# Performance work log

Hardware: AMD Instinct MI355X
Metric: run time of the kernel (lower is better)

## Reference

```python
import jax, jax.numpy as jnp
import numpy as np

EPS = 1e-8
E, H, F, MCL, V = 256, 512, 100, 500, 128000
CTX = MCL - 1  # encoder facts; decoder appends the mean-fact row
NUM_FACTS = 300


def setup_inputs() -> dict:
    key = jax.random.key(0)
    ks = jax.random.split(key, 16)

    def nrm(k, shape, s=0.02):
        return (jax.random.normal(k, shape) * s).astype(jnp.float32)

    return {
        "context": jax.random.randint(ks[0], (CTX, F), 0, V),
        "word_emb": nrm(ks[1], (V, E)),
        "attn1_W": nrm(ks[2], (MCL, E + H)),
        "attn1_b": nrm(ks[3], (MCL,)),
        "attn2_W": nrm(ks[4], (1, MCL)),
        "attn2_b": nrm(ks[5], (1,)),
        "W_ih": nrm(ks[6], (3 * H, 2 * E + F)),
        "W_hh": nrm(ks[7], (3 * H, H)),
        "b_ih": nrm(ks[8], (3 * H,)),
        "b_hh": nrm(ks[9], (3 * H,)),
        "out1_W": nrm(ks[10], (H, E + H)),
        "out1_b": nrm(ks[11], (H,)),
        "out2_W": nrm(ks[12], (V, H)),
        "out2_b": nrm(ks[13], (V,)),
        "h0": jnp.zeros((1, 1, H), jnp.float32),
        "num_facts": NUM_FACTS,
    }


def _encode(context, word_emb):
    # EncoderModule: embedding lookup + PositionalFactEncoder
    emb = word_emb[context]  # [CTX, F, E]
    s = jnp.arange(F, dtype=jnp.float32) / (F - 1)  # slen axis
    e = jnp.arange(E, dtype=jnp.float32) / (E - 1)  # elen axis
    l = 1.0 - s[:, None] - e[None, :] * (1.0 - 2.0 * s[:, None])  # [F, E]
    return jnp.sum(emb * l[None], axis=1)  # [CTX, E]


def reference(context, word_emb, attn1_W, attn1_b, attn2_W, attn2_b,
              W_ih, W_hh, b_ih, b_hh, out1_W, out1_b, out2_W, out2_b,
              h0, num_facts):
    facts = _encode(context, word_emb)  # [CTX, E]
    mean_fact = jnp.mean(facts[:num_facts], axis=0, keepdims=True)  # [1, E]
    fact_embeddings = jnp.concatenate([facts, mean_fact], axis=0)  # [MCL, E]

    # fact-level attention
    h = jnp.broadcast_to(h0.reshape(1, H), (MCL, H))
    attn_in = jnp.concatenate([fact_embeddings, h], axis=1)  # [MCL, E+H]
    e1 = jnp.tanh(attn_in @ attn1_W.T + attn1_b)  # [MCL, MCL]
    energy = (e1 @ attn2_W.T + attn2_b).reshape(1, -1)  # [1, MCL]
    aw = jax.nn.softmax(energy, axis=1)

    # mask: first num_facts ones, zeros, then 1 for the mean/generate slot
    idx = jnp.arange(MCL)
    mask = jnp.where((idx < num_facts) | (idx == MCL - 1), 1.0, 0.0)[None, :]
    aw = aw * mask + EPS
    aw = aw / jnp.sum(aw)
    log_aw = jnp.log(aw)  # [1, MCL]

    attn_weighted_facts = aw @ fact_embeddings  # [1, E]
    f_max_idx = jnp.argmax(aw, axis=1)[0]
    emb_f_max = fact_embeddings[f_max_idx].reshape(1, E)

    # decoder input: embedding of token 1 + zero positional input
    dec_word = word_emb[1].reshape(1, E)
    dec_pos = jnp.zeros((1, F), jnp.float32)
    x = jnp.concatenate([dec_word, dec_pos, emb_f_max], axis=1)  # [1, 2E+F]

    # torch GRU cell (gates ordered r, z, n)
    hprev = h0.reshape(1, H)
    gi = x @ W_ih.T + b_ih
    gh = hprev @ W_hh.T + b_hh
    r = jax.nn.sigmoid(gi[:, :H] + gh[:, :H])
    z = jax.nn.sigmoid(gi[:, H:2 * H] + gh[:, H:2 * H])
    n = jnp.tanh(gi[:, 2 * H:] + r * gh[:, 2 * H:])
    h_new = (1.0 - z) * n + z * hprev  # [1, H]

    # generate branch (f_t == max_context_len - 1): vocab head
    out = jnp.concatenate([h_new, attn_weighted_facts], axis=1)  # [1, H+E]
    out = jax.nn.relu(out @ out1_W.T + out1_b)
    logits = out @ out2_W.T + out2_b  # [1, V]
    y_pred = jax.nn.log_softmax(logits, axis=1)

    decoder_hidden = h_new.reshape(1, 1, H)
    return y_pred, log_aw, decoder_hidden
```

## Files before the change

kernel.cpp:

```cpp
#include <hip/hip_runtime.h>
#include <math.h>

#define E_    256
#define H_    512
#define F_    100
#define MCL_  500
#define CTX_  499
#define V_    128000
#define EPS_  1e-8f

typedef float f4v __attribute__((ext_vector_type(4)));

#define WS_FE      0
#define WS_ENERGY  (WS_FE + MCL_*E_)
#define WS_EBIAS   (WS_ENERGY + MCL_)
#define WS_AWF     (WS_EBIAS + MCL_)
#define WS_FMAX    (WS_AWF + E_)
#define WS_HNEW    (WS_FMAX + E_)
#define WS_ACT     (WS_HNEW + H_)
#define WS_LOGITS  (WS_ACT + H_)
#define WS_BSUM    (WS_LOGITS + V_)
#define WS_CNT     (WS_BSUM + 1024)

__device__ __forceinline__ float wred64(float v) {
#pragma unroll
  for (int o = 32; o; o >>= 1) v += __shfl_xor(v, o, 64);
  return v;
}
__device__ __forceinline__ float qred16(float v) {
#pragma unroll
  for (int o = 8; o; o >>= 1) v += __shfl_xor(v, o, 64);
  return v;
}
__device__ __forceinline__ float dot4(float4 a, float4 b) {
  return a.x*b.x + a.y*b.y + a.z*b.z + a.w*b.w;
}
__device__ __forceinline__ float dot4v(f4v a, f4v b) {
  return a.x*b.x + a.y*b.y + a.z*b.z + a.w*b.w;
}

__global__ __launch_bounds__(256) void k_encode(const int* __restrict__ ctx,
                                                const float* __restrict__ wemb,
                                                float* __restrict__ fe,
                                                const float* __restrict__ a1W,
                                                const float* __restrict__ a1b,
                                                const float* __restrict__ h0,
                                                float* __restrict__ ebias,
                                                int* __restrict__ cnt) {
  __shared__ int toks[2][F_];
  const int t = threadIdx.x;
  if (blockIdx.x >= 250) {
    const int lane = t & 63, sub = lane & 15, grp = lane >> 4;
    const int wid = (blockIdx.x - 250) * 4 + (t >> 6);
    const float4* h4 = (const float4*)h0;
    float4 hr[8];
#pragma unroll
    for (int q = 0; q < 8; ++q) hr[q] = h4[sub + q * 16];
    for (int j0 = wid * 4; j0 < MCL_; j0 += 32 * 4) {
      const int j = j0 + grp;
      if (j < MCL_) {
        const float4* w4 = (const float4*)(a1W + (size_t)j * (E_ + H_) + E_);
        float acc = 0.f;
#pragma unroll
        for (int q = 0; q < 8; ++q) acc += dot4(w4[sub + q * 16], hr[q]);
        acc = qred16(acc);
        if (sub == 0) ebias[j] = acc + a1b[j];
      }
    }
    return;
  }
  if (blockIdx.x == 0 && t == 0) *cnt = 0;
  const int i0 = blockIdx.x * 2;
  const int i1 = i0 + 1;
  if (t < F_) toks[0][t] = ctx[i0 * F_ + t];
  else if (t < 2 * F_) toks[1][t - F_] = (i1 < CTX_) ? ctx[i1 * F_ + (t - F_)] : 0;
  __syncthreads();
  const int row = t >> 7, tt = t & 127;
  const int i = i0 + row;
  const float e0n = (2 * tt) * (1.0f / 255.0f);
  const float e1n = (2 * tt + 1) * (1.0f / 255.0f);
  float x0 = 0.f, y0 = 0.f, x1 = 0.f, y1 = 0.f, x2 = 0.f, y2 = 0.f, x3 = 0.f, y3 = 0.f;
#pragma unroll 5
  for (int f = 0; f < F_; f += 4) {
#pragma unroll
    for (int u = 0; u < 4; ++u) {
      float s = (f + u) * (1.0f / 99.0f);
      float A = 1.0f - s, B = 1.0f - 2.0f * s;
      float l0 = A - e0n * B, l1 = A - e1n * B;
      float2 v = ((const float2*)(wemb + (size_t)toks[row][f + u] * E_))[tt];
      if (u == 0)      { x0 = fmaf(v.x, l0, x0); y0 = fmaf(v.y, l1, y0); }
      else if (u == 1) { x1 = fmaf(v.x, l0, x1); y1 = fmaf(v.y, l1, y1); }
      else if (u == 2) { x2 = fmaf(v.x, l0, x2); y2 = fmaf(v.y, l1, y2); }
      else             { x3 = fmaf(v.x, l0, x3); y3 = fmaf(v.y, l1, y3); }
    }
  }
  if (i < CTX_) {
    float2 r; r.x = (x0 + x1) + (x2 + x3); r.y = (y0 + y1) + (y2 + y3);
    ((float2*)(fe + (size_t)i * E_))[tt] = r;
  }
}

__global__ __launch_bounds__(256) void k_energy(float* __restrict__ fe,
                                                const float* __restrict__ a1W,
                                                const float* __restrict__ ebias,
                                                const float* __restrict__ a2W,
                                                const float* __restrict__ a2b,
                                                const int* __restrict__ nfp,
                                                float* __restrict__ energy,
                                                float* __restrict__ awf,
                                                float* __restrict__ fmaxrow,
                                                float* __restrict__ out_logaw,
                                                int* __restrict__ cnt) {
  __shared__ float sfe[4][E_];
  __shared__ float sred[4][256];
  __shared__ float saw[512];
  __shared__ int sticket;
  const int t = threadIdx.x;
  const int i0 = blockIdx.x * 4;
  const int nf = *nfp;

  if (blockIdx.x == 124) {
    float s0 = 0.f, s1 = 0.f, s2 = 0.f, s3 = 0.f;
    int i = 0;
    for (; i + 4 <= nf; i += 4) {
      s0 += fe[(i + 0) * E_ + t]; s1 += fe[(i + 1) * E_ + t];
      s2 += fe[(i + 2) * E_ + t]; s3 += fe[(i + 3) * E_ + t];
    }
    for (; i < nf; ++i) s0 += fe[i * E_ + t];
    float mv = ((s0 + s1) + (s2 + s3)) / (float)nf;
    sfe[3][t] = mv;
    fe[CTX_ * E_ + t] = mv;
    sfe[0][t] = fe[496 * E_ + t];
    sfe[1][t] = fe[497 * E_ + t];
    sfe[2][t] = fe[498 * E_ + t];
  } else {
#pragma unroll
    for (int r = 0; r < 4; ++r) sfe[r][t] = fe[(i0 + r) * E_ + t];
  }
  __syncthreads();
  float c0 = 0.f, c1 = 0.f, c2 = 0.f, c3 = 0.f;
  const float4* s0p = (const float4*)sfe[0];
  const float4* s1p = (const float4*)sfe[1];
  const float4* s2p = (const float4*)sfe[2];
  const float4* s3p = (const float4*)sfe[3];
  for (int j = t; j < MCL_; j += 256) {
    const float4* w4 = (const float4*)(a1W + (size_t)j * (E_ + H_));
    float d0 = 0.f, d1 = 0.f, d2 = 0.f, d3 = 0.f;
#pragma unroll 8
    for (int q = 0; q < E_ / 4; ++q) {
      float4 a = w4[q];
      d0 += dot4(a, s0p[q]);
      d1 += dot4(a, s1p[q]);
      d2 += dot4(a, s2p[q]);
      d3 += dot4(a, s3p[q]);
    }
    float bj = ebias[j], wj = a2W[j];
    c0 = fmaf(wj, tanhf(d0 + bj), c0);
    c1 = fmaf(wj, tanhf(d1 + bj), c1);
    c2 = fmaf(wj, tanhf(d2 + bj), c2);
    c3 = fmaf(wj, tanhf(d3 + bj), c3);
  }
  sred[0][t] = c0; sred[1][t] = c1; sred[2][t] = c2; sred[3][t] = c3;
  __syncthreads();
  for (int s = 128; s; s >>= 1) {
    if (t < s) {
#pragma unroll
      for (int r = 0; r < 4; ++r) sred[r][t] += sred[r][t + s];
    }
    __syncthreads();
  }
  if (t < 4) energy[i0 + t] = sred[t][0] + a2b[0];

  __threadfence();
  if (t == 0) sticket = atomicAdd(cnt, 1);
  __syncthreads();
  if (sticket != 124) return;
  __threadfence();

  float* red = sred[0];
  int* idx = (int*)sred[1];
  float ev0 = energy[t];
  float ev1 = (t + 256 < MCL_) ? energy[t + 256] : -1e30f;
  red[t] = fmaxf(ev0, ev1); __syncthreads();
  for (int s = 128; s; s >>= 1) { if (t < s) red[t] = fmaxf(red[t], red[t + s]); __syncthreads(); }
  const float mx = red[0]; __syncthreads();

  float p0 = __expf(ev0 - mx);
  float p1 = (t + 256 < MCL_) ? __expf(ev1 - mx) : 0.f;
  red[t] = p0 + p1; __syncthreads();
  for (int s = 128; s; s >>= 1) { if (t < s) red[t] += red[t + s]; __syncthreads(); }
  const float S1 = red[0]; __syncthreads();

  float m0 = ((t < nf) || (t == MCL_ - 1)) ? 1.f : 0.f;
  float m1 = (((t + 256) < nf) || ((t + 256) == MCL_ - 1)) ? 1.f : 0.f;
  float a0 = p0 / S1 * m0 + EPS_;
  float a1 = (t + 256 < MCL_) ? (p1 / S1 * m1 + EPS_) : 0.f;
  red[t] = a0 + a1; __syncthreads();
  for (int s = 128; s; s >>= 1) { if (t < s) red[t] += red[t + s]; __syncthreads(); }
  const float S2 = red[0]; __syncthreads();

  a0 /= S2; a1 /= S2;
  out_logaw[t] = logf(a0);
  if (t + 256 < MCL_) out_logaw[t + 256] = logf(a1);
  saw[t] = a0;
  saw[t + 256] = (t + 256 < MCL_) ? a1 : 0.f;

  float bv; int bi;
  if ((t + 256 < MCL_) && (a1 > a0)) { bv = a1; bi = t + 256; } else { bv = a0; bi = t; }
  red[t] = bv; idx[t] = bi; __syncthreads();
  for (int s = 128; s; s >>= 1) {
    if (t < s) {
      float o = red[t + s]; int oi = idx[t + s];
      if (o > red[t] || (o == red[t] && oi < idx[t])) { red[t] = o; idx[t] = oi; }
    }
    __syncthreads();
  }
  const int fidx = idx[0]; __syncthreads();

  float pa = 0.f, pb = 0.f;
  for (int i2 = 0; i2 < MCL_; i2 += 2) {
    pa = fmaf(saw[i2], fe[i2 * E_ + t], pa);
    pb = fmaf(saw[i2 + 1], fe[(i2 + 1) * E_ + t], pb);
  }
  awf[t] = pa + pb;
  fmaxrow[t] = fe[fidx * E_ + t];
}

__global__ __launch_bounds__(256) void k_gates_gru(const float* __restrict__ Wih,
                                                   const float* __restrict__ bih,
                                                   const float* __restrict__ Whh,
                                                   const float* __restrict__ bhh,
                                                   const float* __restrict__ wemb,
                                                   const float* __restrict__ fmaxrow,
                                                   const float* __restrict__ h0,
                                                   float* __restrict__ hnew,
                                                   float* __restrict__ out_hidden) {
  const int t = threadIdx.x, lane = t & 63, w = t >> 6;
  const int h = blockIdx.x * 4 + w;
  const float4* xa4 = (const float4*)(wemb + E_);
  const float4* xb4 = (const float4*)fmaxrow;
  const float4* h4  = (const float4*)h0;
  float4 xav = xa4[lane], xbv = xb4[lane];
  float4 hva = h4[lane], hvb = h4[lane + 64];
  const float* rr = Wih + (size_t)h * (2 * E_ + F_);
  const float* rz = Wih + (size_t)(H_ + h) * (2 * E_ + F_);
  const float* rn = Wih + (size_t)(2 * H_ + h) * (2 * E_ + F_);
  float gir = dot4(((const float4*)rr)[lane], xav) + dot4(((const float4*)(rr + E_ + F_))[lane], xbv);
  float giz = dot4(((const float4*)rz)[lane], xav) + dot4(((const float4*)(rz + E_ + F_))[lane], xbv);
  float gin = dot4(((const float4*)rn)[lane], xav) + dot4(((const float4*)(rn + E_ + F_))[lane], xbv);
  const float4* wr = (const float4*)(Whh + (size_t)h * H_);
  const float4* wz = (const float4*)(Whh + (size_t)(H_ + h) * H_);
  const float4* wn = (const float4*)(Whh + (size_t)(2 * H_ + h) * H_);
  float ghr = dot4(wr[lane], hva) + dot4(wr[lane + 64], hvb);
  float ghz = dot4(wz[lane], hva) + dot4(wz[lane + 64], hvb);
  float ghn = dot4(wn[lane], hva) + dot4(wn[lane + 64], hvb);
  gir = wred64(gir); giz = wred64(giz); gin = wred64(gin);
  ghr = wred64(ghr); ghz = wred64(ghz); ghn = wred64(ghn);
  if (lane == 0) {
    float r = 1.f / (1.f + __expf(-(gir + bih[h] + ghr + bhh[h])));
    float z = 1.f / (1.f + __expf(-(giz + bih[H_ + h] + ghz + bhh[H_ + h])));
    float n = tanhf(gin + bih[2 * H_ + h] + r * (ghn + bhh[2 * H_ + h]));
    float hv = (1.f - z) * n + z * h0[h];
    hnew[h] = hv;
    out_hidden[h] = hv;
  }
}

__global__ __launch_bounds__(256) void k_out1(const float* __restrict__ o1W,
                                              const float* __restrict__ o1b,
                                              const float* __restrict__ hnew,
                                              const float* __restrict__ awf,
                                              float* __restrict__ act) {
  __shared__ float cat[H_ + E_];
  const int t = threadIdx.x;
#pragma unroll
  for (int idx = t; idx < H_; idx += 256) cat[idx] = hnew[idx];
  cat[H_ + t] = awf[t];
  __syncthreads();
  const int lane = t & 63, sub = lane & 15, grp = lane >> 4;
  const int gw = blockIdx.x * 4 + (t >> 6);
  const float4* c4 = (const float4*)cat;
  const int r = gw * 4 + grp;
  const float4* w4 = (const float4*)(o1W + (size_t)r * (H_ + E_));
  float acc = 0.f;
#pragma unroll
  for (int q = 0; q < 12; ++q) acc += dot4(w4[sub + q * 16], c4[sub + q * 16]);
  acc = qred16(acc);
  if (sub == 0) act[r] = fmaxf(acc + o1b[r], 0.f);
}

__global__ __launch_bounds__(256) void k_vocab(const float* __restrict__ o2W,
                                               const float* __restrict__ o2b,
                                               const float* __restrict__ act,
                                               float* __restrict__ logits,
                                               float* __restrict__ bsum) {
  __shared__ float swsum[4];
  const int t = threadIdx.x;
  const int lane = t & 63, sub = lane & 15, grp = lane >> 4, w = t >> 6;
  const int gw = blockIdx.x * 4 + w;
  const int nW = 1024 * 4;
  const f4v* a4 = (const f4v*)act;
  f4v ar[8];
#pragma unroll
  for (int q = 0; q < 8; ++q) ar[q] = a4[sub + q * 16];
  float sumexp = 0.f;
  for (int v0 = gw * 8; v0 < V_; v0 += nW * 8) {
    const int vA = v0 + grp;
    const int vB = v0 + 4 + grp;
    float accA = 0.f, accB = 0.f;
    if (vB < V_) {
      const f4v* wa = (const f4v*)(o2W + (size_t)vA * H_);
      const f4v* wb = (const f4v*)(o2W + (size_t)vB * H_);
      f4v la[8], lb[8];
#pragma unroll
      for (int q = 0; q < 8; ++q) la[q] = __builtin_nontemporal_load(&wa[sub + q * 16]);
#pragma unroll
      for (int q = 0; q < 8; ++q) lb[q] = __builtin_nontemporal_load(&wb[sub + q * 16]);
#pragma unroll
      for (int q = 0; q < 8; ++q) { accA += dot4v(la[q], ar[q]); accB += dot4v(lb[q], ar[q]); }
    } else if (vA < V_) {
      const f4v* wa = (const f4v*)(o2W + (size_t)vA * H_);
      f4v la[8];
#pragma unroll
      for (int q = 0; q < 8; ++q) la[q] = __builtin_nontemporal_load(&wa[sub + q * 16]);
#pragma unroll
      for (int q = 0; q < 8; ++q) accA += dot4v(la[q], ar[q]);
    }
    accA = qred16(accA);
    accB = qred16(accB);
    if (sub == 0) {
      if (vA < V_) { float lg = accA + o2b[vA]; logits[vA] = lg; sumexp += __expf(lg); }
      if (vB < V_) { float lg = accB + o2b[vB]; logits[vB] = lg; sumexp += __expf(lg); }
    }
  }
  sumexp = wred64(sumexp);
  if (lane == 0) swsum[w] = sumexp;
  __syncthreads();
  if (t == 0) bsum[blockIdx.x] = swsum[0] + swsum[1] + swsum[2] + swsum[3];
}

__global__ __launch_bounds__(256) void k_final(const float* __restrict__ logits,
                                               const float* __restrict__ bsum,
                                               float* __restrict__ y) {
  __shared__ float sr[256];
  const int t = threadIdx.x;
  float s = bsum[t] + bsum[t + 256] + bsum[t + 512] + bsum[t + 768];
  sr[t] = s; __syncthreads();
  for (int o = 128; o; o >>= 1) { if (t < o) sr[t] += sr[t + o]; __syncthreads(); }
  const float lz = logf(sr[0]);
  const int i = blockIdx.x * 256 + t;
  float4 l = ((const float4*)logits)[i];
  ((float4*)y)[i] = make_float4(l.x - lz, l.y - lz, l.z - lz, l.w - lz);
}

extern "C" void kernel_launch(void* const* d_in, const int* in_sizes, int n_in,
                              void* d_out, int out_size, void* d_ws, size_t ws_size,
                              hipStream_t stream) {
  const int*   ctx  = (const int*)d_in[0];
  const float* wemb = (const float*)d_in[1];
  const float* a1W  = (const float*)d_in[2];
  const float* a1b  = (const float*)d_in[3];
  const float* a2W  = (const float*)d_in[4];
  const float* a2b  = (const float*)d_in[5];
  const float* Wih  = (const float*)d_in[6];
  const float* Whh  = (const float*)d_in[7];
  const float* bih  = (const float*)d_in[8];
  const float* bhh  = (const float*)d_in[9];
  const float* o1W  = (const float*)d_in[10];
  const float* o1b  = (const float*)d_in[11];
  const float* o2W  = (const float*)d_in[12];
  const float* o2b  = (const float*)d_in[13];
  const float* h0   = (const float*)d_in[14];
  const int*   nfp  = (const int*)d_in[15];
  float* ws = (float*)d_ws;
  float* y  = (float*)d_out;
  int* cnt = (int*)(ws + WS_CNT);

  k_encode<<<258, 256, 0, stream>>>(ctx, wemb, ws + WS_FE, a1W, a1b, h0,
                                    ws + WS_EBIAS, cnt);
  k_energy<<<125, 256, 0, stream>>>(ws + WS_FE, a1W, ws + WS_EBIAS, a2W, a2b, nfp,
                                    ws + WS_ENERGY, ws + WS_AWF, ws + WS_FMAX,
                                    y + V_, cnt);
  k_gates_gru<<<128, 256, 0, stream>>>(Wih, bih, Whh, bhh, wemb, ws + WS_FMAX, h0,
                                       ws + WS_HNEW, y + V_ + MCL_);
  k_out1<<<32, 256, 0, stream>>>(o1W, o1b, ws + WS_HNEW, ws + WS_AWF, ws + WS_ACT);
  k_vocab<<<1024, 256, 0, stream>>>(o2W, o2b, ws + WS_ACT, ws + WS_LOGITS, ws + WS_BSUM);
  k_final<<<V_ / 1024, 256, 0, stream>>>(ws + WS_LOGITS, ws + WS_BSUM, y);
}
```

Baseline: 127.4 us.

## Split serial mean-fact and attention-weighted sum across extra blocks

```diff
diff --git a/kernel.cpp b/kernel.cpp
--- a/kernel.cpp
+++ b/kernel.cpp
@@ -14,8 +14,10 @@
 #define WS_FE      0
 #define WS_ENERGY  (WS_FE + MCL_*E_)
 #define WS_EBIAS   (WS_ENERGY + MCL_)
-#define WS_AWF     (WS_EBIAS + MCL_)
-#define WS_FMAX    (WS_AWF + E_)
+#define WS_AW      (WS_EBIAS + MCL_)
+#define WS_MEANP   (WS_AW + 512)
+#define WS_AWFP    (WS_MEANP + 8*E_)
+#define WS_FMAX    (WS_AWFP + 8*E_)
 #define WS_HNEW    (WS_FMAX + E_)
 #define WS_ACT     (WS_HNEW + H_)
 #define WS_LOGITS  (WS_ACT + H_)
@@ -46,12 +48,48 @@
                                                 const float* __restrict__ a1b,
                                                 const float* __restrict__ h0,
                                                 float* __restrict__ ebias,
+                                                const int* __restrict__ nfp,
+                                                float* __restrict__ meanp,
                                                 int* __restrict__ cnt) {
-  __shared__ int toks[2][F_];
-  const int t = threadIdx.x;
-  if (blockIdx.x >= 250) {
+  const int t = threadIdx.x;
+  const int b = blockIdx.x;
+
+  if (b >= 258) {
+    const int m = b - 258;
+    const int nf = *nfp;
+    const int chunk = (nf + 7) >> 3;
+    const int lo = m * chunk;
+    const int hi = min(nf, lo + chunk);
+    if (t == 0) {
+      while (atomicAdd(cnt, 0) < 250) __builtin_amdgcn_s_sleep(8);
+    }
+    __syncthreads();
+    __threadfence();
+    float s0 = 0.f, s1 = 0.f, s2 = 0.f, s3 = 0.f;
+    int i = lo;
+    for (; i + 4 <= hi; i += 4) {
+      s0 += fe[(i + 0) * E_ + t]; s1 += fe[(i + 1) * E_ + t];
+      s2 += fe[(i + 2) * E_ + t]; s3 += fe[(i + 3) * E_ + t];
+    }
+    for (; i < hi; ++i) s0 += fe[i * E_ + t];
+    meanp[m * E_ + t] = (s0 + s1) + (s2 + s3);
+    __syncthreads();
+    __threadfence();
+    __shared__ int tick;
+    if (t == 0) tick = atomicAdd(cnt + 1, 1);
+    __syncthreads();
+    if (tick != 7) return;
+    __threadfence();
+    float s = 0.f;
+#pragma unroll
+    for (int q = 0; q < 8; ++q) s += meanp[q * E_ + t];
+    fe[CTX_ * E_ + t] = s / (float)nf;
+    return;
+  }
+
+  if (b >= 250) {
     const int lane = t & 63, sub = lane & 15, grp = lane >> 4;
-    const int wid = (blockIdx.x - 250) * 4 + (t >> 6);
+    const int wid = (b - 250) * 4 + (t >> 6);
     const float4* h4 = (const float4*)h0;
     float4 hr[8];
 #pragma unroll
@@ -69,14 +107,13 @@
     }
     return;
   }
-  if (blockIdx.x == 0 && t == 0) *cnt = 0;
-  const int i0 = blockIdx.x * 2;
-  const int i1 = i0 + 1;
-  if (t < F_) toks[0][t] = ctx[i0 * F_ + t];
-  else if (t < 2 * F_) toks[1][t - F_] = (i1 < CTX_) ? ctx[i1 * F_ + (t - F_)] : 0;
+
+  __shared__ int toks[2][F_];
+  if (t < F_) toks[0][t] = ctx[(b * 2) * F_ + t];
+  else if (t < 2 * F_) toks[1][t - F_] = (b * 2 + 1 < CTX_) ? ctx[(b * 2 + 1) * F_ + (t - F_)] : 0;
   __syncthreads();
   const int row = t >> 7, tt = t & 127;
-  const int i = i0 + row;
+  const int i = b * 2 + row;
   const float e0n = (2 * tt) * (1.0f / 255.0f);
   const float e1n = (2 * tt + 1) * (1.0f / 255.0f);
   float x0 = 0.f, y0 = 0.f, x1 = 0.f, y1 = 0.f, x2 = 0.f, y2 = 0.f, x3 = 0.f, y3 = 0.f;
@@ -86,57 +123,42 @@
     for (int u = 0; u < 4; ++u) {
       float s = (f + u) * (1.0f / 99.0f);
       float A = 1.0f - s, B = 1.0f - 2.0f * s;
-      float l0 = A - e0n * B, l1 = A - e1n * B;
       float2 v = ((const float2*)(wemb + (size_t)toks[row][f + u] * E_))[tt];
-      if (u == 0)      { x0 = fmaf(v.x, l0, x0); y0 = fmaf(v.y, l1, y0); }
-      else if (u == 1) { x1 = fmaf(v.x, l0, x1); y1 = fmaf(v.y, l1, y1); }
-      else if (u == 2) { x2 = fmaf(v.x, l0, x2); y2 = fmaf(v.y, l1, y2); }
-      else             { x3 = fmaf(v.x, l0, x3); y3 = fmaf(v.y, l1, y3); }
+      if (u == 0)      { x0 = fmaf(v.x, A - e0n * B, x0); y0 = fmaf(v.y, A - e1n * B, y0); }
+      else if (u == 1) { x1 = fmaf(v.x, A - e0n * B, x1); y1 = fmaf(v.y, A - e1n * B, y1); }
+      else if (u == 2) { x2 = fmaf(v.x, A - e0n * B, x2); y2 = fmaf(v.y, A - e1n * B, y2); }
+      else             { x3 = fmaf(v.x, A - e0n * B, x3); y3 = fmaf(v.y, A - e1n * B, y3); }
     }
   }
   if (i < CTX_) {
     float2 r; r.x = (x0 + x1) + (x2 + x3); r.y = (y0 + y1) + (y2 + y3);
     ((float2*)(fe + (size_t)i * E_))[tt] = r;
   }
-}
-
-__global__ __launch_bounds__(256) void k_energy(float* __restrict__ fe,
+  __syncthreads();
+  __threadfence();
+  if (t == 0) atomicAdd(cnt, 1);
+}
+
+__global__ __launch_bounds__(256) void k_energy(const float* __restrict__ fe,
                                                 const float* __restrict__ a1W,
                                                 const float* __restrict__ ebias,
                                                 const float* __restrict__ a2W,
                                                 const float* __restrict__ a2b,
                                                 const int* __restrict__ nfp,
                                                 float* __restrict__ energy,
-                                                float* __restrict__ awf,
+                                                float* __restrict__ aw_ws,
                                                 float* __restrict__ fmaxrow,
                                                 float* __restrict__ out_logaw,
                                                 int* __restrict__ cnt) {
   __shared__ float sfe[4][E_];
   __shared__ float sred[4][256];
-  __shared__ float saw[512];
   __shared__ int sticket;
   const int t = threadIdx.x;
   const int i0 = blockIdx.x * 4;
   const int nf = *nfp;
 
-  if (blockIdx.x == 124) {
-    float s0 = 0.f, s1 = 0.f, s2 = 0.f, s3 = 0.f;
-    int i = 0;
-    for (; i + 4 <= nf; i += 4) {
-      s0 += fe[(i + 0) * E_ + t]; s1 += fe[(i + 1) * E_ + t];
-      s2 += fe[(i + 2) * E_ + t]; s3 += fe[(i + 3) * E_ + t];
-    }
-    for (; i < nf; ++i) s0 += fe[i * E_ + t];
-    float mv = ((s0 + s1) + (s2 + s3)) / (float)nf;
-    sfe[3][t] = mv;
-    fe[CTX_ * E_ + t] = mv;
-    sfe[0][t] = fe[496 * E_ + t];
-    sfe[1][t] = fe[497 * E_ + t];
-    sfe[2][t] = fe[498 * E_ + t];
-  } else {
-#pragma unroll
-    for (int r = 0; r < 4; ++r) sfe[r][t] = fe[(i0 + r) * E_ + t];
-  }
+#pragma unroll
+  for (int r = 0; r < 4; ++r) sfe[r][t] = fe[(i0 + r) * E_ + t];
   __syncthreads();
   float c0 = 0.f, c1 = 0.f, c2 = 0.f, c3 = 0.f;
   const float4* s0p = (const float4*)sfe[0];
@@ -171,8 +193,9 @@
   }
   if (t < 4) energy[i0 + t] = sred[t][0] + a2b[0];
 
+  __syncthreads();
   __threadfence();
-  if (t == 0) sticket = atomicAdd(cnt, 1);
+  if (t == 0) sticket = atomicAdd(cnt + 2, 1);
   __syncthreads();
   if (sticket != 124) return;
   __threadfence();
@@ -201,9 +224,8 @@
 
   a0 /= S2; a1 /= S2;
   out_logaw[t] = logf(a0);
-  if (t + 256 < MCL_) out_logaw[t + 256] = logf(a1);
-  saw[t] = a0;
-  saw[t + 256] = (t + 256 < MCL_) ? a1 : 0.f;
+  aw_ws[t] = a0;
+  if (t + 256 < MCL_) { out_logaw[t + 256] = logf(a1); aw_ws[t + 256] = a1; }
 
   float bv; int bi;
   if ((t + 256 < MCL_) && (a1 > a0)) { bv = a1; bi = t + 256; } else { bv = a0; bi = t; }
@@ -216,13 +238,6 @@
     __syncthreads();
   }
   const int fidx = idx[0]; __syncthreads();
-
-  float pa = 0.f, pb = 0.f;
-  for (int i2 = 0; i2 < MCL_; i2 += 2) {
-    pa = fmaf(saw[i2], fe[i2 * E_ + t], pa);
-    pb = fmaf(saw[i2 + 1], fe[(i2 + 1) * E_ + t], pb);
-  }
-  awf[t] = pa + pb;
   fmaxrow[t] = fe[fidx * E_ + t];
 }
 
@@ -233,10 +248,29 @@
                                                    const float* __restrict__ wemb,
                                                    const float* __restrict__ fmaxrow,
                                                    const float* __restrict__ h0,
+                                                   const float* __restrict__ aw,
+                                                   const float* __restrict__ fe,
+                                                   float* __restrict__ awfp,
                                                    float* __restrict__ hnew,
                                                    float* __restrict__ out_hidden) {
-  const int t = threadIdx.x, lane = t & 63, w = t >> 6;
-  const int h = blockIdx.x * 4 + w;
+  const int t = threadIdx.x;
+  const int b = blockIdx.x;
+  if (b >= 128) {
+    const int m = b - 128;
+    const int lo = m * 63;
+    const int hi = min(MCL_, lo + 63);
+    float pa = 0.f, pb = 0.f;
+    int i = lo;
+    for (; i + 2 <= hi; i += 2) {
+      pa = fmaf(aw[i], fe[i * E_ + t], pa);
+      pb = fmaf(aw[i + 1], fe[(i + 1) * E_ + t], pb);
+    }
+    if (i < hi) pa = fmaf(aw[i], fe[i * E_ + t], pa);
+    awfp[m * E_ + t] = pa + pb;
+    return;
+  }
+  const int lane = t & 63, w = t >> 6;
+  const int h = b * 4 + w;
   const float4* xa4 = (const float4*)(wemb + E_);
   const float4* xb4 = (const float4*)fmaxrow;
   const float4* h4  = (const float4*)h0;
@@ -269,13 +303,18 @@
 __global__ __launch_bounds__(256) void k_out1(const float* __restrict__ o1W,
                                               const float* __restrict__ o1b,
                                               const float* __restrict__ hnew,
-                                              const float* __restrict__ awf,
+                                              const float* __restrict__ awfp,
                                               float* __restrict__ act) {
   __shared__ float cat[H_ + E_];
   const int t = threadIdx.x;
 #pragma unroll
   for (int idx = t; idx < H_; idx += 256) cat[idx] = hnew[idx];
-  cat[H_ + t] = awf[t];
+  {
+    float s = 0.f;
+#pragma unroll
+    for (int q = 0; q < 8; ++q) s += awfp[q * E_ + t];
+    cat[H_ + t] = s;
+  }
   __syncthreads();
   const int lane = t & 63, sub = lane & 15, grp = lane >> 4;
   const int gw = blockIdx.x * 4 + (t >> 6);
@@ -376,14 +415,16 @@
   float* y  = (float*)d_out;
   int* cnt = (int*)(ws + WS_CNT);
 
-  k_encode<<<258, 256, 0, stream>>>(ctx, wemb, ws + WS_FE, a1W, a1b, h0,
-                                    ws + WS_EBIAS, cnt);
+  hipMemsetAsync(cnt, 0, 3 * sizeof(int), stream);
+  k_encode<<<266, 256, 0, stream>>>(ctx, wemb, ws + WS_FE, a1W, a1b, h0,
+                                    ws + WS_EBIAS, nfp, ws + WS_MEANP, cnt);
   k_energy<<<125, 256, 0, stream>>>(ws + WS_FE, a1W, ws + WS_EBIAS, a2W, a2b, nfp,
-                                    ws + WS_ENERGY, ws + WS_AWF, ws + WS_FMAX,
+                                    ws + WS_ENERGY, ws + WS_AW, ws + WS_FMAX,
                                     y + V_, cnt);
-  k_gates_gru<<<128, 256, 0, stream>>>(Wih, bih, Whh, bhh, wemb, ws + WS_FMAX, h0,
+  k_gates_gru<<<136, 256, 0, stream>>>(Wih, bih, Whh, bhh, wemb, ws + WS_FMAX, h0,
+                                       ws + WS_AW, ws + WS_FE, ws + WS_AWFP,
                                        ws + WS_HNEW, y + V_ + MCL_);
-  k_out1<<<32, 256, 0, stream>>>(o1W, o1b, ws + WS_HNEW, ws + WS_AWF, ws + WS_ACT);
+  k_out1<<<32, 256, 0, stream>>>(o1W, o1b, ws + WS_HNEW, ws + WS_AWFP, ws + WS_ACT);
   k_vocab<<<1024, 256, 0, stream>>>(o2W, o2b, ws + WS_ACT, ws + WS_LOGITS, ws + WS_BSUM);
   k_final<<<V_ / 1024, 256, 0, stream>>>(ws + WS_LOGITS, ws + WS_BSUM, y);
 }
```

Result: slower. 144.7 us (+13.5%).

## Split attention-weighted fact sum across extra GRU-kernel blocks

Applied to the files above, without the earlier changes.

```diff
diff --git a/kernel.cpp b/kernel.cpp
--- a/kernel.cpp
+++ b/kernel.cpp
@@ -14,8 +14,9 @@
 #define WS_FE      0
 #define WS_ENERGY  (WS_FE + MCL_*E_)
 #define WS_EBIAS   (WS_ENERGY + MCL_)
-#define WS_AWF     (WS_EBIAS + MCL_)
-#define WS_FMAX    (WS_AWF + E_)
+#define WS_AW      (WS_EBIAS + MCL_)
+#define WS_AWFP    (WS_AW + 512)
+#define WS_FMAX    (WS_AWFP + 8*E_)
 #define WS_HNEW    (WS_FMAX + E_)
 #define WS_ACT     (WS_HNEW + H_)
 #define WS_LOGITS  (WS_ACT + H_)
@@ -86,12 +87,11 @@
     for (int u = 0; u < 4; ++u) {
       float s = (f + u) * (1.0f / 99.0f);
       float A = 1.0f - s, B = 1.0f - 2.0f * s;
-      float l0 = A - e0n * B, l1 = A - e1n * B;
       float2 v = ((const float2*)(wemb + (size_t)toks[row][f + u] * E_))[tt];
-      if (u == 0)      { x0 = fmaf(v.x, l0, x0); y0 = fmaf(v.y, l1, y0); }
-      else if (u == 1) { x1 = fmaf(v.x, l0, x1); y1 = fmaf(v.y, l1, y1); }
-      else if (u == 2) { x2 = fmaf(v.x, l0, x2); y2 = fmaf(v.y, l1, y2); }
-      else             { x3 = fmaf(v.x, l0, x3); y3 = fmaf(v.y, l1, y3); }
+      if (u == 0)      { x0 = fmaf(v.x, A - e0n * B, x0); y0 = fmaf(v.y, A - e1n * B, y0); }
+      else if (u == 1) { x1 = fmaf(v.x, A - e0n * B, x1); y1 = fmaf(v.y, A - e1n * B, y1); }
+      else if (u == 2) { x2 = fmaf(v.x, A - e0n * B, x2); y2 = fmaf(v.y, A - e1n * B, y2); }
+      else             { x3 = fmaf(v.x, A - e0n * B, x3); y3 = fmaf(v.y, A - e1n * B, y3); }
     }
   }
   if (i < CTX_) {
@@ -107,13 +107,12 @@
                                                 const float* __restrict__ a2b,
                                                 const int* __restrict__ nfp,
                                                 float* __restrict__ energy,
-                                                float* __restrict__ awf,
+                                                float* __restrict__ aw_ws,
                                                 float* __restrict__ fmaxrow,
                                                 float* __restrict__ out_logaw,
                                                 int* __restrict__ cnt) {
   __shared__ float sfe[4][E_];
   __shared__ float sred[4][256];
-  __shared__ float saw[512];
   __shared__ int sticket;
   const int t = threadIdx.x;
   const int i0 = blockIdx.x * 4;
@@ -201,9 +200,8 @@
 
   a0 /= S2; a1 /= S2;
   out_logaw[t] = logf(a0);
-  if (t + 256 < MCL_) out_logaw[t + 256] = logf(a1);
-  saw[t] = a0;
-  saw[t + 256] = (t + 256 < MCL_) ? a1 : 0.f;
+  aw_ws[t] = a0;
+  if (t + 256 < MCL_) { out_logaw[t + 256] = logf(a1); aw_ws[t + 256] = a1; }
 
   float bv; int bi;
   if ((t + 256 < MCL_) && (a1 > a0)) { bv = a1; bi = t + 256; } else { bv = a0; bi = t; }
@@ -216,13 +214,6 @@
     __syncthreads();
   }
   const int fidx = idx[0]; __syncthreads();
-
-  float pa = 0.f, pb = 0.f;
-  for (int i2 = 0; i2 < MCL_; i2 += 2) {
-    pa = fmaf(saw[i2], fe[i2 * E_ + t], pa);
-    pb = fmaf(saw[i2 + 1], fe[(i2 + 1) * E_ + t], pb);
-  }
-  awf[t] = pa + pb;
   fmaxrow[t] = fe[fidx * E_ + t];
 }
 
@@ -233,10 +224,29 @@
                                                    const float* __restrict__ wemb,
                                                    const float* __restrict__ fmaxrow,
                                                    const float* __restrict__ h0,
+                                                   const float* __restrict__ aw,
+                                                   const float* __restrict__ fe,
+                                                   float* __restrict__ awfp,
                                                    float* __restrict__ hnew,
                                                    float* __restrict__ out_hidden) {
-  const int t = threadIdx.x, lane = t & 63, w = t >> 6;
-  const int h = blockIdx.x * 4 + w;
+  const int t = threadIdx.x;
+  const int b = blockIdx.x;
+  if (b >= 128) {
+    const int m = b - 128;
+    const int lo = m * 63;
+    const int hi = min(MCL_, lo + 63);
+    float pa = 0.f, pb = 0.f;
+    int i = lo;
+    for (; i + 2 <= hi; i += 2) {
+      pa = fmaf(aw[i], fe[i * E_ + t], pa);
+      pb = fmaf(aw[i + 1], fe[(i + 1) * E_ + t], pb);
+    }
+    if (i < hi) pa = fmaf(aw[i], fe[i * E_ + t], pa);
+    awfp[m * E_ + t] = pa + pb;
+    return;
+  }
+  const int lane = t & 63, w = t >> 6;
+  const int h = b * 4 + w;
   const float4* xa4 = (const float4*)(wemb + E_);
   const float4* xb4 = (const float4*)fmaxrow;
   const float4* h4  = (const float4*)h0;
@@ -269,13 +279,18 @@
 __global__ __launch_bounds__(256) void k_out1(const float* __restrict__ o1W,
                                               const float* __restrict__ o1b,
                                               const float* __restrict__ hnew,
-                                              const float* __restrict__ awf,
+                                              const float* __restrict__ awfp,
                                               float* __restrict__ act) {
   __shared__ float cat[H_ + E_];
   const int t = threadIdx.x;
 #pragma unroll
   for (int idx = t; idx < H_; idx += 256) cat[idx] = hnew[idx];
-  cat[H_ + t] = awf[t];
+  {
+    float s = 0.f;
+#pragma unroll
+    for (int q = 0; q < 8; ++q) s += awfp[q * E_ + t];
+    cat[H_ + t] = s;
+  }
   __syncthreads();
   const int lane = t & 63, sub = lane & 15, grp = lane >> 4;
   const int gw = blockIdx.x * 4 + (t >> 6);
@@ -379,11 +394,12 @@
   k_encode<<<258, 256, 0, stream>>>(ctx, wemb, ws + WS_FE, a1W, a1b, h0,
                                     ws + WS_EBIAS, cnt);
   k_energy<<<125, 256, 0, stream>>>(ws + WS_FE, a1W, ws + WS_EBIAS, a2W, a2b, nfp,
-                                    ws + WS_ENERGY, ws + WS_AWF, ws + WS_FMAX,
+                                    ws + WS_ENERGY, ws + WS_AW, ws + WS_FMAX,
                                     y + V_, cnt);
-  k_gates_gru<<<128, 256, 0, stream>>>(Wih, bih, Whh, bhh, wemb, ws + WS_FMAX, h0,
+  k_gates_gru<<<136, 256, 0, stream>>>(Wih, bih, Whh, bhh, wemb, ws + WS_FMAX, h0,
+                                       ws + WS_AW, ws + WS_FE, ws + WS_AWFP,
                                        ws + WS_HNEW, y + V_ + MCL_);
-  k_out1<<<32, 256, 0, stream>>>(o1W, o1b, ws + WS_HNEW, ws + WS_AWF, ws + WS_ACT);
+  k_out1<<<32, 256, 0, stream>>>(o1W, o1b, ws + WS_HNEW, ws + WS_AWFP, ws + WS_ACT);
   k_vocab<<<1024, 256, 0, stream>>>(o2W, o2b, ws + WS_ACT, ws + WS_LOGITS, ws + WS_BSUM);
   k_final<<<V_ / 1024, 256, 0, stream>>>(ws + WS_LOGITS, ws + WS_BSUM, y);
 }
```

New measurement: 125.3 us. Within noise of the previous version (-1.7%).
